# Optimization experiments

Measured on AMD Instinct MI355X. Metric: run time of the kernel, lower is better.

The kernel has to match this reference:

```python
import jax, jax.numpy as jnp
import numpy as np
from jax import lax

N_KERNELS = 200
FILT = 13
POOL = 6
RNN_H = 100
N_HEADS = 8
HEAD_D = 32
MH_SIZE = 100
BN_EPS = 1e-5


def _conv_bn_pool(x, w, gamma, beta, mean, var):
    # x: [B,4,L], w: [200,4,13]; VALID conv -> BN(eval) -> ReLU -> MaxPool1d(6)
    y = lax.conv_general_dilated(x, w, (1,), 'VALID',
                                 dimension_numbers=('NCH', 'OIH', 'NCH'))
    inv = gamma / jnp.sqrt(var + BN_EPS)
    y = y * inv[None, :, None] + (beta - mean * inv)[None, :, None]
    y = jax.nn.relu(y)
    L = y.shape[-1]
    P = (L // POOL) * POOL
    y = y[..., :P].reshape(y.shape[0], y.shape[1], P // POOL, POOL).max(-1)
    return y  # dropout is identity in eval


def _bilstm(x, w_ih, w_hh, b_ih, b_hh):
    # x: [B,S,200]; weights: [n_layers=2, n_dirs=2, 4H, in] / [2,2,4H,H] / [2,2,4H]
    xs = jnp.swapaxes(x, 0, 1)  # [S,B,in]
    B = xs.shape[1]

    def run(xseq, wi, wh, bi, bh, reverse):
        def step(carry, xt):
            h, c = carry
            g = xt @ wi.T + h @ wh.T + (bi + bh)
            i, f, gg, o = jnp.split(g, 4, axis=-1)  # torch gate order i,f,g,o
            c = jax.nn.sigmoid(f) * c + jax.nn.sigmoid(i) * jnp.tanh(gg)
            h = jax.nn.sigmoid(o) * jnp.tanh(c)
            return (h, c), h
        init = (jnp.zeros((B, RNN_H), xseq.dtype), jnp.zeros((B, RNN_H), xseq.dtype))
        _, hs = lax.scan(step, init, xseq, reverse=reverse)
        return hs

    for l in range(w_ih.shape[0]):
        hf = run(xs, w_ih[l, 0], w_hh[l, 0], b_ih[l, 0], b_hh[l, 0], False)
        hb = run(xs, w_ih[l, 1], w_hh[l, 1], b_ih[l, 1], b_hh[l, 1], True)
        xs = jnp.concatenate([hf, hb], -1)
    return jnp.swapaxes(xs, 0, 1)  # [B,S,2H]


def setup_inputs() -> dict:
    key = jax.random.key(0)
    ks = jax.random.split(key, 24)
    B = 16
    D = 2 * RNN_H  # 200
    inp = {
        'input_p': jax.random.normal(ks[0], (B, 4, 3000), jnp.float32),
        'input_e': jax.random.normal(ks[1], (B, 4, 2000), jnp.float32),
        'conv_p_w': jax.random.normal(ks[2], (N_KERNELS, 4, FILT), jnp.float32) * 0.1,
        'bn_p_gamma': jnp.ones((N_KERNELS,), jnp.float32),
        'bn_p_beta': jnp.zeros((N_KERNELS,), jnp.float32),
        'bn_p_mean': jnp.zeros((N_KERNELS,), jnp.float32),
        'bn_p_var': jnp.ones((N_KERNELS,), jnp.float32),
        'conv_e_w': jax.random.normal(ks[3], (N_KERNELS, 4, FILT), jnp.float32) * 0.1,
        'bn_e_gamma': jnp.ones((N_KERNELS,), jnp.float32),
        'bn_e_beta': jnp.zeros((N_KERNELS,), jnp.float32),
        'bn_e_mean': jnp.zeros((N_KERNELS,), jnp.float32),
        'bn_e_var': jnp.ones((N_KERNELS,), jnp.float32),
        # biLSTM: both layers have input dim 200 (layer0: conv feats; layer1: 2*H)
        'lstm_w_ih': jax.random.normal(ks[4], (2, 2, 4 * RNN_H, D), jnp.float32) * 0.05,
        'lstm_w_hh': jax.random.normal(ks[5], (2, 2, 4 * RNN_H, RNN_H), jnp.float32) * 0.05,
        'lstm_b_ih': jax.random.normal(ks[6], (2, 2, 4 * RNN_H), jnp.float32) * 0.05,
        'lstm_b_hh': jax.random.normal(ks[7], (2, 2, 4 * RNN_H), jnp.float32) * 0.05,
        'wq': jax.random.normal(ks[8], (N_HEADS, D, HEAD_D), jnp.float32) * 0.07,
        'bq': jax.random.normal(ks[9], (N_HEADS, HEAD_D), jnp.float32) * 0.07,
        'wk': jax.random.normal(ks[10], (N_HEADS, D, HEAD_D), jnp.float32) * 0.07,
        'bk': jax.random.normal(ks[11], (N_HEADS, HEAD_D), jnp.float32) * 0.07,
        'wv': jax.random.normal(ks[12], (N_HEADS, D, HEAD_D), jnp.float32) * 0.07,
        'bv': jax.random.normal(ks[13], (N_HEADS, HEAD_D), jnp.float32) * 0.07,
        'mh_w': jax.random.normal(ks[14], (N_HEADS * HEAD_D, MH_SIZE), jnp.float32) * 0.06,
        'mh_b': jax.random.normal(ks[15], (MH_SIZE,), jnp.float32) * 0.06,
        'fc3_w': jax.random.normal(ks[16], (MH_SIZE, 2), jnp.float32) * 0.1,
        'fc3_b': jax.random.normal(ks[17], (2,), jnp.float32) * 0.1,
    }
    return inp


def reference(input_p, input_e, conv_p_w, bn_p_gamma, bn_p_beta, bn_p_mean, bn_p_var,
              conv_e_w, bn_e_gamma, bn_e_beta, bn_e_mean, bn_e_var,
              lstm_w_ih, lstm_w_hh, lstm_b_ih, lstm_b_hh,
              wq, bq, wk, bk, wv, bv, mh_w, mh_b, fc3_w, fc3_b):
    p = _conv_bn_pool(input_p, conv_p_w, bn_p_gamma, bn_p_beta, bn_p_mean, bn_p_var)  # [B,200,498]
    e = _conv_bn_pool(input_e, conv_e_w, bn_e_gamma, bn_e_beta, bn_e_mean, bn_e_var)  # [B,200,331]
    out = jnp.concatenate([p, e], axis=2)                 # [B,200,829]
    out = jnp.transpose(out, (0, 2, 1))                   # [B,S,200]
    out = _bilstm(out, lstm_w_ih, lstm_w_hh, lstm_b_ih, lstm_b_hh)  # [B,S,200]
    # (F_RNN/R_RNN split + re-concat in torch is an identity; eval dropout = identity)
    q = jnp.einsum('bsd,hdk->bhsk', out, wq) + bq[None, :, None, :]
    k = jnp.einsum('bsd,hdk->bhsk', out, wk) + bk[None, :, None, :]
    v = jnp.einsum('bsd,hdk->bhsk', out, wv) + bv[None, :, None, :]
    scale = 1.0 / np.sqrt(HEAD_D).astype(np.float32)
    scores = jnp.einsum('bhsk,bhtk->bhst', q, k) * scale
    p_attn = jax.nn.softmax(scores, axis=-1)              # [B,H,S,S]
    attn = jax.nn.relu(jnp.einsum('bhst,bhtv->bhsv', p_attn, v))
    B, H, S, K = attn.shape
    attn_cat = jnp.transpose(attn, (0, 2, 1, 3)).reshape(B, S, H * K)   # head-major concat
    h = jax.nn.relu(attn_cat @ mh_w + mh_b)               # [B,S,100]
    r = h.sum(axis=1)                                     # [B,100]
    r = (r - r.mean()) / jnp.std(r, ddof=1)               # torch std is unbiased
    probs = jax.nn.softmax(r @ fc3_w + fc3_b, axis=1)     # [B,2]
    pAttn_concat = jnp.transpose(p_attn, (0, 2, 1, 3)).reshape(B, S, H * S)
    return probs, pAttn_concat
```

## Files before the change

kernel.cpp:

```cpp
#include <hip/hip_runtime.h>

#define S_TOT 829
#define SP 498
#define BATCH 16
#define NK 200
#define RH 100
#define DMODEL 200
#define G4 400
#define MROWS (BATCH*S_TOT)
#define CTS 32
#define PTILES 16
#define ETILES 11

using v8s = __attribute__((ext_vector_type(8))) short;
using v4f = __attribute__((ext_vector_type(4))) float;

__device__ inline v4f mfma16(v8s a, v8s b, v4f c){
    return __builtin_amdgcn_mfma_f32_16x16x32_bf16(a, b, c, 0, 0, 0);
}
__device__ inline unsigned short f2bf(float f){
    unsigned int u = __float_as_uint(f);
    unsigned int r = (u + 0x7FFFu + ((u >> 16) & 1u)) >> 16;
    return (unsigned short)r;
}
__device__ inline float sigf(float x){ return 1.0f/(1.0f + exp2f(-1.44269504f*x)); }
__device__ inline float tanhfast(float x){ return 2.0f/(1.0f + exp2f(-2.88539008f*x)) - 1.0f; }

__global__ void prep(const float* __restrict__ w_ih, const float* __restrict__ w_hh,
                     const float* __restrict__ b_ih, const float* __restrict__ b_hh,
                     const float* __restrict__ wq, const float* __restrict__ bq,
                     const float* __restrict__ wk, const float* __restrict__ bk,
                     const float* __restrict__ wv, const float* __restrict__ bv,
                     const float* __restrict__ mh_w,
                     unsigned short* __restrict__ WihBf, float* __restrict__ bias2,
                     unsigned short* __restrict__ WhhBf, unsigned short* __restrict__ wqkvT,
                     float* __restrict__ qkvBias, unsigned short* __restrict__ mhwT)
{
    int t = blockIdx.x*blockDim.x + threadIdx.x;
    if (t < 320000) { WihBf[t] = f2bf(w_ih[t]); }
    else if (t < 323200) { int i = t-320000; bias2[i] = b_ih[i] + b_hh[i]; }
    else if (t < 483200) { int i = t-323200; WhhBf[i] = f2bf(w_hh[i]); }
    else if (t < 636800) { int i = t-483200; int r = i/200, d = i%200;
        int which = r>>8, hh = (r>>5)&7, j = r&31;
        const float* ws = which==0?wq:(which==1?wk:wv);
        wqkvT[i] = f2bf(ws[(hh*200 + d)*32 + j]); }
    else if (t < 637568) { int r = t-636800; int which = r>>8, hh=(r>>5)&7, j=r&31;
        const float* bs = which==0?bq:(which==1?bk:bv);
        qkvBias[r] = bs[hh*32 + j]; }
    else if (t < 663168) { int i = t-637568; int n = i/256, k = i%256;
        mhwT[i] = f2bf(mh_w[k*100 + n]); }
}

__global__ __launch_bounds__(256) void conv_pool(
    const float* __restrict__ xp, const float* __restrict__ xe,
    const float* __restrict__ wp, const float* __restrict__ gp, const float* __restrict__ bp,
    const float* __restrict__ mp, const float* __restrict__ vp,
    const float* __restrict__ we, const float* __restrict__ ge, const float* __restrict__ be,
    const float* __restrict__ me, const float* __restrict__ ve,
    unsigned short* __restrict__ Xbf)
{
    __shared__ float wlds[NK*52];
    __shared__ float xlds[4][CTS*6 + 12];
    int tile = blockIdx.x, b = blockIdx.y;
    const float *x, *w, *g, *bb, *mm, *vv; int L, S, st, sbase;
    if (tile < PTILES){ x=xp; w=wp; g=gp; bb=bp; mm=mp; vv=vp; L=3000; S=SP;      st=tile*CTS;          sbase=0;  }
    else              { x=xe; w=we; g=ge; bb=be; mm=me; vv=ve; L=2000; S=S_TOT-SP; st=(tile-PTILES)*CTS; sbase=SP; }
    int tid = threadIdx.x;
    int scount = min(CTS, S - st);
    int r0 = st*6;
    int ext = scount*6 + 12;

    for (int i = tid; i < NK*52; i += 256) wlds[i] = w[i];
    for (int i = tid; i < 4*ext; i += 256){
        int ic = i/ext, j = i%ext;
        xlds[ic][j] = x[(long)b*4*L + ic*L + r0 + j];
    }
    __syncthreads();

    int oc = tid;
    if (oc < NK){
        float wreg[52];
        #pragma unroll
        for (int j=0;j<52;++j) wreg[j] = wlds[oc*52 + j];
        float inv = g[oc] * rsqrtf(vv[oc] + 1e-5f);
        float sh  = bb[oc] - mm[oc]*inv;
        for (int sl = 0; sl < scount; ++sl){
            float xw[4][18];
            #pragma unroll
            for (int ic=0;ic<4;++ic)
                #pragma unroll
                for (int j=0;j<18;++j) xw[ic][j] = xlds[ic][sl*6 + j];
            float best = -1e30f;
            #pragma unroll
            for (int u=0; u<6; ++u){
                float a = 0.f;
                #pragma unroll
                for (int ic=0; ic<4; ++ic)
                    #pragma unroll
                    for (int k=0; k<13; ++k) a += xw[ic][u+k] * wreg[ic*13+k];
                best = fmaxf(best, a*inv + sh);
            }
            Xbf[((long)b*S_TOT + sbase + st + sl)*NK + oc] = f2bf(fmaxf(best, 0.f));
        }
    }
}

__global__ __launch_bounds__(256) void gemm_bf16(
    const unsigned short* __restrict__ A, const unsigned short* __restrict__ B,
    const float* __restrict__ bias, float* __restrict__ C, unsigned short* __restrict__ Cbf,
    int M, int N, int K, long strideB, long strideBias, long strideC, int relu)
{
    __shared__ unsigned short As[64][40];
    __shared__ unsigned short Bs[64][40];
    int tid = threadIdx.x;
    int m0 = blockIdx.x*64, n0 = blockIdx.y*64, z = blockIdx.z;
    const unsigned short* Bz = B + z*strideB;
    const float* biasz = bias + z*strideBias;
    float* Cz = C + z*strideC;
    unsigned short* Cbz = Cbf ? Cbf + z*strideC : nullptr;

    int lane = tid & 63, wave = tid >> 6;
    int wm = wave >> 1, wn = wave & 1;
    int quad = lane >> 4, lc = lane & 15;
    int row = tid >> 2, seg = tid & 3;

    v4f acc[2][2];
    #pragma unroll
    for (int i=0;i<2;++i)
      #pragma unroll
      for (int j=0;j<2;++j) acc[i][j] = (v4f){0.f,0.f,0.f,0.f};

    int KC = (K + 31) >> 5;
    for (int kc = 0; kc < KC; ++kc){
        int k0 = kc << 5;
        __syncthreads();
        {
            int gm = m0 + row, gn = n0 + row, ks = k0 + seg*8;
            if (gm < M && ks + 8 <= K)
                *(v8s*)&As[row][seg*8] = *(const v8s*)(A + (long)gm*K + ks);
            else
                for (int j=0;j<8;++j) As[row][seg*8+j] = (gm<M && ks+j<K) ? A[(long)gm*K+ks+j] : 0;
            if (gn < N && ks + 8 <= K)
                *(v8s*)&Bs[row][seg*8] = *(const v8s*)(Bz + (long)gn*K + ks);
            else
                for (int j=0;j<8;++j) Bs[row][seg*8+j] = (gn<N && ks+j<K) ? Bz[(long)gn*K+ks+j] : 0;
        }
        __syncthreads();
        v8s a0 = *(const v8s*)&As[wm*32 + lc][quad*8];
        v8s a1 = *(const v8s*)&As[wm*32 + 16 + lc][quad*8];
        v8s b0 = *(const v8s*)&Bs[wn*32 + lc][quad*8];
        v8s b1 = *(const v8s*)&Bs[wn*32 + 16 + lc][quad*8];
        acc[0][0] = mfma16(a0, b0, acc[0][0]);
        acc[0][1] = mfma16(a0, b1, acc[0][1]);
        acc[1][0] = mfma16(a1, b0, acc[1][0]);
        acc[1][1] = mfma16(a1, b1, acc[1][1]);
    }
    #pragma unroll
    for (int i=0;i<2;++i)
      #pragma unroll
      for (int j=0;j<2;++j){
        int nc = n0 + wn*32 + j*16 + lc;
        #pragma unroll
        for (int r=0;r<4;++r){
            int mr = m0 + wm*32 + i*16 + quad*4 + r;
            if (mr < M && nc < N){
                float v = acc[i][j][r] + biasz[nc];
                if (relu) v = fmaxf(v, 0.f);
                Cz[(long)mr*N + nc] = v;
                if (Cbz) Cbz[(long)mr*N + nc] = f2bf(v);
            }
        }
      }
}

__global__ __launch_bounds__(512) void lstm_scan(
    const float* __restrict__ gx, const unsigned short* __restrict__ whh,
    unsigned short* __restrict__ Hout)
{
    __shared__ unsigned short h_bf[16][136];
    __shared__ float gates[2][408];
    int tid = threadIdx.x;
    int dir = blockIdx.x >> 3, bg = blockIdx.x & 7;
    int b0 = bg*2;
    int lane = tid & 63, wave = tid >> 6;
    int quad = lane >> 4, lc = lane & 15;

    for (int idx = tid; idx < 16*136; idx += 512) ((unsigned short*)h_bf)[idx] = 0;

    const unsigned short* W = whh + dir*G4*RH;
    v8s bfr[4][4];
    #pragma unroll
    for (int i=0;i<4;++i){
        int nt = wave + 8*i;
        #pragma unroll
        for (int kc=0;kc<4;++kc){
            v8s v;
            #pragma unroll
            for (int j=0;j<8;++j){
                int n = nt*16 + lc, k = kc*32 + quad*8 + j;
                v[j] = (nt<25 && k<RH) ? (short)W[n*RH + k] : (short)0;
            }
            bfr[i][kc] = v;
        }
    }
    bool act = tid < 200;
    int b_l = tid/100, nn = tid%100;
    long gbase = (((long)dir*BATCH + (b0+b_l))*S_TOT)*(long)G4 + nn;
    float creg = 0.f;

    float gA[4], gB[4];
    auto loadg = [&](float (&g)[4], int t){
        if (act && t < S_TOT){
            int s = dir ? (S_TOT-1-t) : t;
            const float* gp = gx + gbase + (long)s*G4;
            g[0] = gp[0]; g[1] = gp[100]; g[2] = gp[200]; g[3] = gp[300];
        }
    };
    loadg(gA, 0);
    loadg(gB, 1);
    __syncthreads();

    auto bar = [&](){
        asm volatile("s_waitcnt lgkmcnt(0)" ::: "memory");
        __builtin_amdgcn_s_barrier();
    };

    auto step = [&](int t, float (&g)[4]){
        int s = dir ? (S_TOT-1-t) : t;
        v8s afr[4];
        #pragma unroll
        for (int kc=0;kc<4;++kc)
            afr[kc] = *(const v8s*)&h_bf[lc][kc*32 + quad*8];
        #pragma unroll
        for (int i=0;i<4;++i){
            int nt = wave + 8*i;
            if (nt < 25){
                v4f d0 = (v4f){0.f,0.f,0.f,0.f}, d1 = (v4f){0.f,0.f,0.f,0.f};
                d0 = mfma16(afr[0], bfr[i][0], d0);
                d1 = mfma16(afr[1], bfr[i][1], d1);
                d0 = mfma16(afr[2], bfr[i][2], d0);
                d1 = mfma16(afr[3], bfr[i][3], d1);
                if (lane < 16){
                    gates[0][nt*16+lc] = d0[0] + d1[0];
                    gates[1][nt*16+lc] = d0[1] + d1[1];
                }
            }
        }
        bar();
        if (act){
            float gi = gates[b_l][nn]     + g[0];
            float gf = gates[b_l][100+nn] + g[1];
            float gg = gates[b_l][200+nn] + g[2];
            float go = gates[b_l][300+nn] + g[3];
            creg = sigf(gf)*creg + sigf(gi)*tanhfast(gg);
            float h = sigf(go) * tanhfast(creg);
            unsigned short hb = f2bf(h);
            h_bf[b_l][nn] = hb;
            Hout[((long)(b0+b_l)*S_TOT + s)*DMODEL + dir*RH + nn] = hb;
        }
        loadg(g, t+2);
        bar();
    };

    for (int t=0; t+1 < S_TOT; t += 2){
        step(t,   gA);
        step(t+1, gB);
    }
    step(S_TOT-1, gA);
}

__global__ __launch_bounds__(256) void attn_fused(
    const unsigned short* __restrict__ qkvbf, const float* __restrict__ qkvf,
    float* __restrict__ outP, unsigned short* __restrict__ attn_cat)
{
    __shared__ unsigned short P_lds[16][840];
    __shared__ float redbuf[4][16];
    __shared__ float attnbuf[4][16][17];
    int tid = threadIdx.x;
    int lane = tid & 63, wave = tid >> 6;
    int quad = lane >> 4, lc = lane & 15;
    int b = blockIdx.y >> 3, h = blockIdx.y & 7;
    int s0 = blockIdx.x*16;
    const float scale = 0.17677669529663687f;

    v8s aq = (v8s){0,0,0,0,0,0,0,0};
    int sg = s0 + lc;
    if (sg < S_TOT) aq = *(const v8s*)(qkvbf + ((long)(b*S_TOT + sg))*768 + h*32 + quad*8);

    v4f frag[13];
    #pragma unroll
    for (int i=0;i<13;++i){
        int tg = (i*4 + wave)*16 + lc;
        v8s bk = (v8s){0,0,0,0,0,0,0,0};
        if (tg < S_TOT) bk = *(const v8s*)(qkvbf + ((long)(b*S_TOT + tg))*768 + 256 + h*32 + quad*8);
        v4f z = (v4f){0.f,0.f,0.f,0.f};
        frag[i] = mfma16(aq, bk, z);
    }
    float mx[4] = {-1e30f,-1e30f,-1e30f,-1e30f};
    #pragma unroll
    for (int i=0;i<13;++i){
        int tcol = (i*4+wave)*16 + lc;
        bool tv = tcol < S_TOT;
        #pragma unroll
        for (int r=0;r<4;++r){
            float x = tv ? frag[i][r]*scale : -1e30f;
            frag[i][r] = x;
            mx[r] = fmaxf(mx[r], x);
        }
    }
    #pragma unroll
    for (int off=1; off<16; off<<=1)
        #pragma unroll
        for (int r=0;r<4;++r) mx[r] = fmaxf(mx[r], __shfl_xor(mx[r], off));
    if (lc == 0){ redbuf[wave][quad*4+0]=mx[0]; redbuf[wave][quad*4+1]=mx[1];
                  redbuf[wave][quad*4+2]=mx[2]; redbuf[wave][quad*4+3]=mx[3]; }
    __syncthreads();
    float M4[4], sm[4] = {0.f,0.f,0.f,0.f};
    #pragma unroll
    for (int r=0;r<4;++r){
        int rr = quad*4+r;
        M4[r] = fmaxf(fmaxf(redbuf[0][rr], redbuf[1][rr]), fmaxf(redbuf[2][rr], redbuf[3][rr]));
    }
    #pragma unroll
    for (int i=0;i<13;++i)
        #pragma unroll
        for (int r=0;r<4;++r){
            float e = exp2f((frag[i][r] - M4[r]) * 1.44269504f);
            frag[i][r] = e; sm[r] += e;
        }
    #pragma unroll
    for (int off=1; off<16; off<<=1)
        #pragma unroll
        for (int r=0;r<4;++r) sm[r] += __shfl_xor(sm[r], off);
    __syncthreads();
    if (lc == 0){ redbuf[wave][quad*4+0]=sm[0]; redbuf[wave][quad*4+1]=sm[1];
                  redbuf[wave][quad*4+2]=sm[2]; redbuf[wave][quad*4+3]=sm[3]; }
    __syncthreads();
    float inv[4];
    #pragma unroll
    for (int r=0;r<4;++r){
        int rr = quad*4+r;
        inv[r] = 1.0f / (redbuf[0][rr]+redbuf[1][rr]+redbuf[2][rr]+redbuf[3][rr]);
    }
    #pragma unroll
    for (int i=0;i<13;++i){
        int tloc = (i*4+wave)*16 + lc;
        #pragma unroll
        for (int r=0;r<4;++r){
            float p = frag[i][r] * inv[r];
            int srow = quad*4 + r;
            P_lds[srow][tloc] = f2bf(p);
            int sgr = s0 + srow;
            if (sgr < S_TOT && tloc < S_TOT)
                outP[32 + (((long)b*S_TOT + sgr)*8 + h)*S_TOT + tloc] = p;
        }
    }
    __syncthreads();
    int jt = wave & 1;
    v4f dacc = (v4f){0.f,0.f,0.f,0.f};
    #pragma unroll
    for (int i=0;i<13;++i){
        int ch = (wave>>1) + 2*i;
        v8s ap = *(const v8s*)&P_lds[lc][ch*32 + quad*8];
        v8s bv;
        #pragma unroll
        for (int j=0;j<8;++j){
            int t = ch*32 + quad*8 + j;
            float vv = (t < S_TOT) ? qkvf[((long)(b*S_TOT + t))*768 + 512 + h*32 + jt*16 + lc] : 0.f;
            bv[j] = (short)f2bf(vv);
        }
        dacc = mfma16(ap, bv, dacc);
    }
    #pragma unroll
    for (int r=0;r<4;++r) attnbuf[wave][quad*4+r][lc] = dacc[r];
    __syncthreads();
    for (int idx = tid; idx < 512; idx += 256){
        int sr = idx >> 5, j = idx & 31;
        float v = attnbuf[j>>4][sr][j&15] + attnbuf[2+(j>>4)][sr][j&15];
        v = fmaxf(v, 0.f);
        if (s0 + sr < S_TOT)
            attn_cat[((long)(b*S_TOT + s0 + sr))*256 + h*32 + j] = f2bf(v);
    }
}

__global__ void rowsum_partial(const float* __restrict__ h2, float* __restrict__ part)
{
    int b = blockIdx.x, cch = blockIdx.y, i = threadIdx.x;
    if (i >= 100) return;
    int sBeg = cch*104, sEnd = min(S_TOT, sBeg+104);
    float acc = 0.f;
    for (int s = sBeg; s < sEnd; ++s) acc += h2[((long)b*S_TOT + s)*100 + i];
    part[(b*8 + cch)*100 + i] = acc;
}

__global__ __launch_bounds__(256) void final_head(
    const float* __restrict__ part, const float* __restrict__ fc3w,
    const float* __restrict__ fc3b, float* __restrict__ outp)
{
    __shared__ float r_lds[1600];
    __shared__ float wred[2][4];
    int tid = threadIdx.x;
    float lsum = 0.f, lsq = 0.f;
    for (int idx = tid; idx < 1600; idx += 256){
        int b = idx/100, i = idx%100;
        float s = 0.f;
        for (int c=0;c<8;++c) s += part[(b*8+c)*100 + i];
        r_lds[idx] = s;
        lsum += s; lsq += s*s;
    }
    #pragma unroll
    for (int off=32; off>=1; off>>=1){
        lsum += __shfl_xor(lsum, off);
        lsq  += __shfl_xor(lsq, off);
    }
    int wave = tid >> 6;
    if ((tid & 63) == 0){ wred[0][wave] = lsum; wred[1][wave] = lsq; }
    __syncthreads();
    float S1 = wred[0][0]+wred[0][1]+wred[0][2]+wred[0][3];
    float S2 = wred[1][0]+wred[1][1]+wred[1][2]+wred[1][3];
    float mean = S1/1600.0f;
    float var = (S2 - S1*mean)/1599.0f;
    float isd = rsqrtf(var);
    if (tid < 16){
        float l0 = fc3b[0], l1 = fc3b[1];
        for (int i=0;i<100;++i){
            float rn = (r_lds[tid*100+i] - mean)*isd;
            l0 += rn * fc3w[i*2+0];
            l1 += rn * fc3w[i*2+1];
        }
        float m = fmaxf(l0, l1);
        float e0 = exp2f((l0-m)*1.44269504f), e1 = exp2f((l1-m)*1.44269504f);
        float d = e0 + e1;
        outp[tid*2+0] = e0/d;
        outp[tid*2+1] = e1/d;
    }
}

extern "C" void kernel_launch(void* const* d_in, const int* in_sizes, int n_in,
                              void* d_out, int out_size, void* d_ws, size_t ws_size,
                              hipStream_t stream)
{
    const float* input_p = (const float*)d_in[0];
    const float* input_e = (const float*)d_in[1];
    const float* conv_p_w = (const float*)d_in[2];
    const float* bn_p_g = (const float*)d_in[3];
    const float* bn_p_b = (const float*)d_in[4];
    const float* bn_p_m = (const float*)d_in[5];
    const float* bn_p_v = (const float*)d_in[6];
    const float* conv_e_w = (const float*)d_in[7];
    const float* bn_e_g = (const float*)d_in[8];
    const float* bn_e_b = (const float*)d_in[9];
    const float* bn_e_m = (const float*)d_in[10];
    const float* bn_e_v = (const float*)d_in[11];
    const float* lstm_w_ih = (const float*)d_in[12];
    const float* lstm_w_hh = (const float*)d_in[13];
    const float* lstm_b_ih = (const float*)d_in[14];
    const float* lstm_b_hh = (const float*)d_in[15];
    const float* wq = (const float*)d_in[16];
    const float* bq = (const float*)d_in[17];
    const float* wk = (const float*)d_in[18];
    const float* bk = (const float*)d_in[19];
    const float* wv = (const float*)d_in[20];
    const float* bv = (const float*)d_in[21];
    const float* mh_w = (const float*)d_in[22];
    const float* mh_b = (const float*)d_in[23];
    const float* fc3_w = (const float*)d_in[24];
    const float* fc3_b = (const float*)d_in[25];
    float* out = (float*)d_out;

    char* ws = (char*)d_ws;
    size_t off = 0;
    auto alloc = [&](size_t bytes)->char*{
        char* p = ws + off; off += (bytes + 255) & ~(size_t)255; return p;
    };
    unsigned short* Xbf   = (unsigned short*)alloc((size_t)MROWS*200*2);
    float*          gatex = (float*)alloc((size_t)2*MROWS*400*4);
    unsigned short* H0bf  = (unsigned short*)alloc((size_t)MROWS*200*2);
    unsigned short* OUTbf = (unsigned short*)alloc((size_t)MROWS*200*2);
    unsigned short* QKVbf = (unsigned short*)alloc((size_t)MROWS*768*2);
    unsigned short* attnc = (unsigned short*)alloc((size_t)MROWS*256*2);
    float*          h2    = (float*)alloc((size_t)MROWS*100*4);
    float*          part  = (float*)alloc((size_t)16*8*100*4);
    unsigned short* WihBf = (unsigned short*)alloc(320000*2);
    float*          bias2 = (float*)alloc(3200*4);
    unsigned short* WhhBf = (unsigned short*)alloc(160000*2);
    unsigned short* wqkvT = (unsigned short*)alloc(153600*2);
    float*          qkvBias = (float*)alloc(768*4);
    unsigned short* mhwT  = (unsigned short*)alloc(25600*2);
    (void)ws_size; (void)in_sizes; (void)n_in; (void)out_size;

    prep<<<(663168+255)/256, 256, 0, stream>>>(lstm_w_ih, lstm_w_hh, lstm_b_ih, lstm_b_hh,
        wq, bq, wk, bk, wv, bv, mh_w, WihBf, bias2, WhhBf, wqkvT, qkvBias, mhwT);

    conv_pool<<<dim3(PTILES+ETILES, BATCH), 256, 0, stream>>>(input_p, input_e,
        conv_p_w, bn_p_g, bn_p_b, bn_p_m, bn_p_v,
        conv_e_w, bn_e_g, bn_e_b, bn_e_m, bn_e_v, Xbf);

    dim3 gGate((MROWS+63)/64, (400+63)/64, 2);
    gemm_bf16<<<gGate, 256, 0, stream>>>(Xbf, WihBf, bias2, gatex, nullptr,
        MROWS, 400, 200, (long)400*200, 400, (long)MROWS*400, 0);
    lstm_scan<<<16, 512, 0, stream>>>(gatex, WhhBf, H0bf);

    gemm_bf16<<<gGate, 256, 0, stream>>>(H0bf, WihBf + 2*400*200, bias2 + 800, gatex, nullptr,
        MROWS, 400, 200, (long)400*200, 400, (long)MROWS*400, 0);
    lstm_scan<<<16, 512, 0, stream>>>(gatex, WhhBf + 2*400*100, OUTbf);

    float* QKVf = gatex;
    dim3 gQKV((MROWS+63)/64, 768/64, 1);
    gemm_bf16<<<gQKV, 256, 0, stream>>>(OUTbf, wqkvT, qkvBias, QKVf, QKVbf,
        MROWS, 768, 200, 0, 0, 0, 0);

    dim3 gAttn(52, 128);
    attn_fused<<<gAttn, 256, 0, stream>>>(QKVbf, QKVf, out, attnc);

    dim3 gMh((MROWS+63)/64, (100+63)/64, 1);
    gemm_bf16<<<gMh, 256, 0, stream>>>(attnc, mhwT, mh_b, h2, nullptr,
        MROWS, 100, 256, 0, 0, 0, 1);

    rowsum_partial<<<dim3(16,8), 128, 0, stream>>>(h2, part);
    final_head<<<1, 256, 0, stream>>>(part, fc3_w, fc3_b, out);
}
```

Baseline: 1.874 ms.

## Interleave LSTM W_hh gate rows so each wave owns its cell updates, one barrier per step

The recurrent weight matrix is permuted in prep so that each 16-column MFMA tile holds all four gates (i,f,g,o) for four hidden units. Each wave can then finish the cell update for its own units from a private LDS scratch, with no block-wide exchange of gate values. The hidden state is double-buffered in LDS, so one barrier per timestep replaces two on the serial recurrence. In exchange the activation work is spread across lanes of many waves, the weight layout is more complex, and the writes to Hout become more scattered.

```diff
diff --git a/kernel.cpp b/kernel.cpp
--- a/kernel.cpp
+++ b/kernel.cpp
@@ -39,7 +39,12 @@
     int t = blockIdx.x*blockDim.x + threadIdx.x;
     if (t < 320000) { WihBf[t] = f2bf(w_ih[t]); }
     else if (t < 323200) { int i = t-320000; bias2[i] = b_ih[i] + b_hh[i]; }
-    else if (t < 483200) { int i = t-323200; WhhBf[i] = f2bf(w_hh[i]); }
+    else if (t < 483200) { int i = t-323200;
+        int blk = i/40000, rem = i%40000;
+        int p = rem/100, k = rem%100;
+        int nt = p>>4, lcp = p&15;
+        int n = 4*nt + (lcp>>2), g = lcp&3;
+        WhhBf[i] = f2bf(w_hh[blk*40000 + (g*100+n)*100 + k]); }
     else if (t < 636800) { int i = t-483200; int r = i/200, d = i%200;
         int which = r>>8, hh = (r>>5)&7, j = r&31;
         const float* ws = which==0?wq:(which==1?wk:wv);
@@ -177,15 +182,15 @@
     const float* __restrict__ gx, const unsigned short* __restrict__ whh,
     unsigned short* __restrict__ Hout)
 {
-    __shared__ unsigned short h_bf[16][136];
-    __shared__ float gates[2][408];
+    __shared__ unsigned short h_bf[2][16][136];
+    __shared__ float scratch[8][4][2][16];
     int tid = threadIdx.x;
     int dir = blockIdx.x >> 3, bg = blockIdx.x & 7;
     int b0 = bg*2;
     int lane = tid & 63, wave = tid >> 6;
     int quad = lane >> 4, lc = lane & 15;
 
-    for (int idx = tid; idx < 16*136; idx += 512) ((unsigned short*)h_bf)[idx] = 0;
+    for (int idx = tid; idx < 2*16*136; idx += 512) ((unsigned short*)h_bf)[idx] = 0;
 
     const unsigned short* W = whh + dir*G4*RH;
     v8s bfr[4][4];
@@ -203,14 +208,17 @@
             bfr[i][kc] = v;
         }
     }
-    bool act = tid < 200;
-    int b_l = tid/100, nn = tid%100;
-    long gbase = (((long)dir*BATCH + (b0+b_l))*S_TOT)*(long)G4 + nn;
+
+    int tl = lane >> 3, uu = (lane >> 1) & 3, bl = lane & 1;
+    int myNt = wave + 8*tl;
+    bool actv = (lane < 32) && (myNt < 25);
+    int nu = 4*myNt + uu;
+    long gbase = (((long)dir*BATCH + (b0+bl))*S_TOT)*(long)G4 + nu;
     float creg = 0.f;
 
     float gA[4], gB[4];
     auto loadg = [&](float (&g)[4], int t){
-        if (act && t < S_TOT){
+        if (actv && t < S_TOT){
             int s = dir ? (S_TOT-1-t) : t;
             const float* gp = gx + gbase + (long)s*G4;
             g[0] = gp[0]; g[1] = gp[100]; g[2] = gp[200]; g[3] = gp[300];
@@ -220,17 +228,13 @@
     loadg(gB, 1);
     __syncthreads();
 
-    auto bar = [&](){
-        asm volatile("s_waitcnt lgkmcnt(0)" ::: "memory");
-        __builtin_amdgcn_s_barrier();
-    };
-
     auto step = [&](int t, float (&g)[4]){
         int s = dir ? (S_TOT-1-t) : t;
+        int pp = t & 1;
         v8s afr[4];
         #pragma unroll
         for (int kc=0;kc<4;++kc)
-            afr[kc] = *(const v8s*)&h_bf[lc][kc*32 + quad*8];
+            afr[kc] = *(const v8s*)&h_bf[pp][lc][kc*32 + quad*8];
         #pragma unroll
         for (int i=0;i<4;++i){
             int nt = wave + 8*i;
@@ -241,25 +245,28 @@
                 d0 = mfma16(afr[2], bfr[i][2], d0);
                 d1 = mfma16(afr[3], bfr[i][3], d1);
                 if (lane < 16){
-                    gates[0][nt*16+lc] = d0[0] + d1[0];
-                    gates[1][nt*16+lc] = d0[1] + d1[1];
+                    scratch[wave][i][0][lc] = d0[0] + d1[0];
+                    scratch[wave][i][1][lc] = d0[1] + d1[1];
                 }
             }
         }
-        bar();
-        if (act){
-            float gi = gates[b_l][nn]     + g[0];
-            float gf = gates[b_l][100+nn] + g[1];
-            float gg = gates[b_l][200+nn] + g[2];
-            float go = gates[b_l][300+nn] + g[3];
+        asm volatile("s_waitcnt lgkmcnt(0)" ::: "memory");
+        __builtin_amdgcn_sched_barrier(0);
+        if (actv){
+            v4f gt = *(const v4f*)&scratch[wave][tl][bl][4*uu];
+            float gi = gt[0] + g[0];
+            float gf = gt[1] + g[1];
+            float gg = gt[2] + g[2];
+            float go = gt[3] + g[3];
             creg = sigf(gf)*creg + sigf(gi)*tanhfast(gg);
             float h = sigf(go) * tanhfast(creg);
             unsigned short hb = f2bf(h);
-            h_bf[b_l][nn] = hb;
-            Hout[((long)(b0+b_l)*S_TOT + s)*DMODEL + dir*RH + nn] = hb;
+            h_bf[pp^1][bl][nu] = hb;
+            Hout[((long)(b0+bl)*S_TOT + s)*DMODEL + dir*RH + nu] = hb;
         }
         loadg(g, t+2);
-        bar();
+        asm volatile("s_waitcnt lgkmcnt(0)" ::: "memory");
+        __builtin_amdgcn_s_barrier();
     };
 
     for (int t=0; t+1 < S_TOT; t += 2){
```

After: 2.034 ms. 1.09x slower.
